# Performance work log

Hardware: AMD Instinct MI355X
Metric: run time of the kernel (lower is better)

## Reference

```python
import jax, jax.numpy as jnp
import numpy as np

N_NODES = 100000
N_EDGES = 1600000
IN_F = 64
H1_F = 64
N_CLS = 16
NEG_SLOPE = 0.01  # F.leaky_relu default


def _sage_pool(x, src, dst, n_nodes, W_pool, b_pool, W_self, W_neigh, bias):
    """DGL SAGEConv with aggregator_type='pool'.
    msg = relu(x[src] @ W_pool + b_pool); pooled = max over in-edges per dst
    out = x @ W_self + pooled @ W_neigh + bias (empty segments pooled to 0)."""
    m = jax.nn.relu(x[src] @ W_pool + b_pool)                 # [E, d_in]
    pooled = jax.ops.segment_max(m, dst, num_segments=n_nodes)  # [N, d_in]
    deg = jax.ops.segment_sum(jnp.ones(dst.shape[0], x.dtype), dst,
                              num_segments=n_nodes)           # [N]
    pooled = jnp.where(deg[:, None] > 0, pooled, jnp.zeros((), x.dtype))
    return x @ W_self + pooled @ W_neigh + bias               # [N, d_out]


def setup_inputs() -> dict:
    key = jax.random.key(0)
    ks = jax.random.split(key, 12)
    sc_in = 1.0 / np.sqrt(IN_F)
    sc_h1 = 1.0 / np.sqrt(H1_F)
    inp = {
        "in_feat": jax.random.normal(ks[0], (N_NODES, IN_F), jnp.float32),
        "src": jax.random.randint(ks[1], (N_EDGES,), 0, N_NODES),
        "dst": jax.random.randint(ks[2], (N_EDGES,), 0, N_NODES),
        # layer 1 (in=64 -> out=64)
        "W_pool1": jax.random.normal(ks[3], (IN_F, IN_F), jnp.float32) * sc_in,
        "b_pool1": jnp.zeros((IN_F,), jnp.float32),
        "W_self1": jax.random.normal(ks[4], (IN_F, H1_F), jnp.float32) * sc_in,
        "W_neigh1": jax.random.normal(ks[5], (IN_F, H1_F), jnp.float32) * sc_in,
        "bias1": jnp.zeros((H1_F,), jnp.float32),
        # layer 2 (in=64 -> out=16)
        "W_pool2": jax.random.normal(ks[6], (H1_F, H1_F), jnp.float32) * sc_h1,
        "b_pool2": jnp.zeros((H1_F,), jnp.float32),
        "W_self2": jax.random.normal(ks[7], (H1_F, N_CLS), jnp.float32) * sc_h1,
        "W_neigh2": jax.random.normal(ks[8], (H1_F, N_CLS), jnp.float32) * sc_h1,
        "bias2": jnp.zeros((N_CLS,), jnp.float32),
    }
    return inp


def reference(in_feat, src, dst,
              W_pool1, b_pool1, W_self1, W_neigh1, bias1,
              W_pool2, b_pool2, W_self2, W_neigh2, bias2):
    n = in_feat.shape[0]
    h = _sage_pool(in_feat, src, dst, n, W_pool1, b_pool1, W_self1, W_neigh1, bias1)
    h = jnp.where(h >= 0, h, NEG_SLOPE * h)  # leaky_relu
    out = _sage_pool(h, src, dst, n, W_pool2, b_pool2, W_self2, W_neigh2, bias2)
    return out
```

## Files before the change

### kernel.cpp

```cpp
#include <hip/hip_runtime.h>
#include <cstddef>
#include <cstdint>

#define CAP 64
#define SCAP 40
#define CHUNK2 4096
#define PR 5632
#define HPR 2816

typedef _Float16 h2 __attribute__((ext_vector_type(2)));
static __device__ __forceinline__ h2 h2max(h2 a, h2 b) {
  return __builtin_elementwise_max(a, b);
}
static __device__ __forceinline__ h2 bch2(int u) { return __builtin_bit_cast(h2, u); }
static __device__ __forceinline__ int packrelu(float a, float b) {
  h2 t; t.x = (_Float16)fmaxf(a, 0.f); t.y = (_Float16)fmaxf(b, 0.f);
  return __builtin_bit_cast(int, t);
}
static __device__ __forceinline__ int packleaky(float a, float b) {
  float la = (a >= 0.f) ? a : 0.01f * a;
  float lb = (b >= 0.f) ? b : 0.01f * b;
  h2 t; t.x = (_Float16)la; t.y = (_Float16)lb;
  return __builtin_bit_cast(int, t);
}
static __device__ __forceinline__ float fdot2f(h2 a, h2 b, float c) {
#if __has_builtin(__builtin_amdgcn_fdot2)
  return __builtin_amdgcn_fdot2(a, b, c, false);
#else
  return c + (float)a.x * (float)b.x + (float)a.y * (float)b.y;
#endif
}

static __device__ __forceinline__ void stageW64(h2* dstLds,
                                                const float* __restrict__ W,
                                                int tid) {
  #pragma unroll
  for (int it = 0; it < 2; it++) {
    int idx = it * 256 + tid;
    int kp = idx >> 4;
    int c4 = idx & 15;
    float4 a = ((const float4*)(W + (2 * kp) * 64))[c4];
    float4 b = ((const float4*)(W + (2 * kp + 1) * 64))[c4];
    h2 h0; h0.x = (_Float16)a.x; h0.y = (_Float16)b.x;
    h2 h1; h1.x = (_Float16)a.y; h1.y = (_Float16)b.y;
    h2 hv; hv.x = (_Float16)a.z; hv.y = (_Float16)b.z;
    h2 h3; h3.x = (_Float16)a.w; h3.y = (_Float16)b.w;
    int4 o = make_int4(__builtin_bit_cast(int, h0), __builtin_bit_cast(int, h1),
                       __builtin_bit_cast(int, hv), __builtin_bit_cast(int, h3));
    *(int4*)(dstLds + kp * 64 + c4 * 4) = o;
  }
}

__global__ __launch_bounds__(256) void k_build(const int* __restrict__ src,
                                               const int* __restrict__ dst,
                                               unsigned int* __restrict__ pairs,
                                               int* __restrict__ cnt2,
                                               int E, int P, int NC,
                                               const float* __restrict__ X,
                                               const float* __restrict__ W,
                                               const float* __restrict__ bias,
                                               _Float16* __restrict__ Z, int n) {
  __shared__ __attribute__((aligned(16))) char smem[24576];
  int tid = threadIdx.x;
  if ((int)blockIdx.x < NC) {
    int* hcnt = (int*)smem;
    for (int p = tid; p < 512; p += 256) hcnt[p] = 0;
    __syncthreads();
    int chunk = blockIdx.x;
    int e0 = chunk * CHUNK2;
    unsigned int* pbase = pairs + (size_t)chunk * P * SCAP;
    #pragma unroll
    for (int k = 0; k < CHUNK2 / 256; k++) {
      int e = e0 + k * 256 + tid;
      if (e < E) {
        int d = dst[e], s = src[e];
        int p = d >> 8;
        int slot = atomicAdd(&hcnt[p], 1);
        if (slot < SCAP)
          pbase[p * SCAP + slot] = (unsigned)s | ((unsigned)(d & 255) << 17);
      }
    }
    __syncthreads();
    int* cbase = cnt2 + (size_t)chunk * P;
    for (int p = tid; p < P; p += 256) {
      int c = hcnt[p];
      cbase[p] = (c < SCAP) ? c : SCAP;
    }
    return;
  }
  h2* sW  = (h2*)smem;
  h2* sXT = (h2*)(smem + 8192);
  stageW64(sW, W, tid);
  int node0 = (blockIdx.x - NC) * 128;
  #pragma unroll
  for (int it = 0; it < 8; it++) {
    int idx = it * 256 + tid;
    int row = idx & 127, c4 = idx >> 7;
    int node = node0 + row;
    float4 v = make_float4(0.f, 0.f, 0.f, 0.f);
    if (node < n) v = ((const float4*)(X + (size_t)node * 64))[c4];
    h2 a; a.x = (_Float16)v.x; a.y = (_Float16)v.y;
    h2 d; d.x = (_Float16)v.z; d.y = (_Float16)v.w;
    sXT[(2 * c4 + 0) * 128 + row] = a;
    sXT[(2 * c4 + 1) * 128 + row] = d;
  }
  __syncthreads();
  int lane = tid & 63;
  int cg = tid >> 6;
  float acc0[16], acc1[16];
  #pragma unroll
  for (int c4 = 0; c4 < 4; c4++) {
    float4 bv = ((const float4*)bias)[cg * 4 + c4];
    acc0[c4 * 4 + 0] = bv.x; acc0[c4 * 4 + 1] = bv.y;
    acc0[c4 * 4 + 2] = bv.z; acc0[c4 * 4 + 3] = bv.w;
    acc1[c4 * 4 + 0] = bv.x; acc1[c4 * 4 + 1] = bv.y;
    acc1[c4 * 4 + 2] = bv.z; acc1[c4 * 4 + 3] = bv.w;
  }
  #pragma unroll 8
  for (int kp = 0; kp < 32; kp++) {
    h2 x0 = sXT[kp * 128 + lane];
    h2 x1 = sXT[kp * 128 + lane + 64];
    const int4* wq = (const int4*)(sW + kp * 64 + cg * 16);
    #pragma unroll
    for (int q4 = 0; q4 < 4; q4++) {
      int4 wv = wq[q4];
      h2 w0 = bch2(wv.x), w1 = bch2(wv.y), w2 = bch2(wv.z), w3 = bch2(wv.w);
      acc0[q4 * 4 + 0] = fdot2f(x0, w0, acc0[q4 * 4 + 0]);
      acc0[q4 * 4 + 1] = fdot2f(x0, w1, acc0[q4 * 4 + 1]);
      acc0[q4 * 4 + 2] = fdot2f(x0, w2, acc0[q4 * 4 + 2]);
      acc0[q4 * 4 + 3] = fdot2f(x0, w3, acc0[q4 * 4 + 3]);
      acc1[q4 * 4 + 0] = fdot2f(x1, w0, acc1[q4 * 4 + 0]);
      acc1[q4 * 4 + 1] = fdot2f(x1, w1, acc1[q4 * 4 + 1]);
      acc1[q4 * 4 + 2] = fdot2f(x1, w2, acc1[q4 * 4 + 2]);
      acc1[q4 * 4 + 3] = fdot2f(x1, w3, acc1[q4 * 4 + 3]);
    }
  }
  int nodeA = node0 + lane;
  int nodeB = node0 + lane + 64;
  if (nodeA < n) {
    int4 o0, o1;
    o0.x = packrelu(acc0[0], acc0[1]);   o0.y = packrelu(acc0[2], acc0[3]);
    o0.z = packrelu(acc0[4], acc0[5]);   o0.w = packrelu(acc0[6], acc0[7]);
    o1.x = packrelu(acc0[8], acc0[9]);   o1.y = packrelu(acc0[10], acc0[11]);
    o1.z = packrelu(acc0[12], acc0[13]); o1.w = packrelu(acc0[14], acc0[15]);
    char* rp = (char*)Z + (size_t)nodeA * 128 + cg * 32;
    ((int4*)rp)[0] = o0; ((int4*)rp)[1] = o1;
  }
  if (nodeB < n) {
    int4 o0, o1;
    o0.x = packrelu(acc1[0], acc1[1]);   o0.y = packrelu(acc1[2], acc1[3]);
    o0.z = packrelu(acc1[4], acc1[5]);   o0.w = packrelu(acc1[6], acc1[7]);
    o1.x = packrelu(acc1[8], acc1[9]);   o1.y = packrelu(acc1[10], acc1[11]);
    o1.z = packrelu(acc1[12], acc1[13]); o1.w = packrelu(acc1[14], acc1[15]);
    char* rp = (char*)Z + (size_t)nodeB * 128 + cg * 32;
    ((int4*)rp)[0] = o0; ((int4*)rp)[1] = o1;
  }
}

__global__ __launch_bounds__(256) void k_fill3(const unsigned int* __restrict__ pairs,
                                               const int* __restrict__ cnt2,
                                               int* __restrict__ rowcnt,
                                               int* __restrict__ bucket,
                                               int n, int NC, int P) {
  __shared__ int sbucket[128 * CAP];
  __shared__ int scnt[128];
  __shared__ int soff[256];
  __shared__ int scnt2[512];
  int tid = threadIdx.x;
  int p = blockIdx.x >> 1;
  int half = blockIdx.x & 1;
  if (tid < 128) scnt[tid] = 0;
  for (int c = tid; c < NC; c += 256) scnt2[c] = cnt2[(size_t)c * P + p];
  __syncthreads();
  int total = NC * SCAP;
  for (int t = tid; t < total; t += 256) {
    int chunk = t / SCAP;
    int slot = t - chunk * SCAP;
    if (slot < scnt2[chunk]) {
      unsigned int u = pairs[(size_t)chunk * P * SCAP + p * SCAP + slot];
      int dlow = (int)(u >> 17);
      if ((dlow >> 7) == half) {
        int s = (int)(u & 0x1FFFFu);
        int li = dlow & 127;
        int sl = atomicAdd(&scnt[li], 1);
        if (sl < CAP)
          sbucket[li * CAP + sl] = s;
      }
    }
  }
  __syncthreads();
  int c = 0;
  if (tid < 128) {
    c = scnt[tid];
    if (c > CAP) c = CAP;
  }
  int ca = (c + 3) & ~3;
  soff[tid] = (tid < 128) ? ca : 0;
  __syncthreads();
  #pragma unroll
  for (int off = 1; off < 256; off <<= 1) {
    int t = (tid >= off) ? soff[tid - off] : 0;
    __syncthreads();
    soff[tid] += t;
    __syncthreads();
  }
  if (tid < 128) {
    int local = soff[tid] - ca;
    int node = (p << 8) + (half << 7) + tid;
    int gbase = p * PR + half * HPR + local;
    if (node < n)
      rowcnt[node] = gbase | (c << 22);
    for (int j = 0; j < c; j += 4) {
      int4 v = *(const int4*)&sbucket[tid * CAP + j];
      *(int4*)&bucket[gbase + j] = v;
    }
  }
}

static __device__ __forceinline__ h2 gather_one(const char* zb,
                                                const int* __restrict__ bucket,
                                                int rc) {
  int c = rc >> 22;
  const int* bk = bucket + (rc & 0x3FFFFF);
  h2 acc = (h2)(_Float16)0;
  int j = 0;
  for (; j + 8 <= c; j += 8) {
    int4 a = *(const int4*)(bk + j);
    int4 d = *(const int4*)(bk + j + 4);
    int u0 = *(const int*)(zb + (size_t)a.x * 128);
    int u1 = *(const int*)(zb + (size_t)a.y * 128);
    int u2 = *(const int*)(zb + (size_t)a.z * 128);
    int u3 = *(const int*)(zb + (size_t)a.w * 128);
    int u4 = *(const int*)(zb + (size_t)d.x * 128);
    int u5 = *(const int*)(zb + (size_t)d.y * 128);
    int u6 = *(const int*)(zb + (size_t)d.z * 128);
    int u7 = *(const int*)(zb + (size_t)d.w * 128);
    h2 m0 = h2max(bch2(u0), bch2(u1));
    h2 m1 = h2max(bch2(u2), bch2(u3));
    h2 m2 = h2max(bch2(u4), bch2(u5));
    h2 m3 = h2max(bch2(u6), bch2(u7));
    acc = h2max(acc, h2max(h2max(m0, m1), h2max(m2, m3)));
  }
  if (j + 4 <= c) {
    int4 a = *(const int4*)(bk + j);
    int u0 = *(const int*)(zb + (size_t)a.x * 128);
    int u1 = *(const int*)(zb + (size_t)a.y * 128);
    int u2 = *(const int*)(zb + (size_t)a.z * 128);
    int u3 = *(const int*)(zb + (size_t)a.w * 128);
    acc = h2max(acc, h2max(h2max(bch2(u0), bch2(u1)), h2max(bch2(u2), bch2(u3))));
    j += 4;
  }
  if (j + 2 <= c) {
    int2 a = *(const int2*)(bk + j);
    int u0 = *(const int*)(zb + (size_t)a.x * 128);
    int u1 = *(const int*)(zb + (size_t)a.y * 128);
    acc = h2max(acc, h2max(bch2(u0), bch2(u1)));
    j += 2;
  }
  if (j < c) {
    int u0 = *(const int*)(zb + (size_t)bk[j] * 128);
    acc = h2max(acc, bch2(u0));
  }
  return acc;
}

__global__ __launch_bounds__(256) void k_gather2(const _Float16* __restrict__ Z,
                                                 const int* __restrict__ bucket,
                                                 const int* __restrict__ rowcnt,
                                                 _Float16* __restrict__ pooled, int n) {
  int t = blockIdx.x * 256 + threadIdx.x;
  int pairid = t >> 5;
  int sub = t & 31;
  int nA = pairid * 2;
  int nB = nA + 1;
  if (nA >= n) return;
  const char* zb = (const char*)Z + sub * 4;
  int rcA = rowcnt[nA];
  h2 accA, accB;
  if (nB < n) {
    int rcB = rowcnt[nB];
    accA = gather_one(zb, bucket, rcA);
    accB = gather_one(zb, bucket, rcB);
    *(int*)((char*)pooled + (size_t)nA * 128 + sub * 4) = __builtin_bit_cast(int, accA);
    *(int*)((char*)pooled + (size_t)nB * 128 + sub * 4) = __builtin_bit_cast(int, accB);
  } else {
    accA = gather_one(zb, bucket, rcA);
    *(int*)((char*)pooled + (size_t)nA * 128 + sub * 4) = __builtin_bit_cast(int, accA);
  }
}

__global__ __launch_bounds__(256) void k_hl(const float* __restrict__ X,
                                            const _Float16* __restrict__ P,
                                            const float* __restrict__ Ws,
                                            const float* __restrict__ Wn,
                                            const float* __restrict__ bias,
                                            const float* __restrict__ Wp2,
                                            const float* __restrict__ bp2,
                                            _Float16* __restrict__ H,
                                            _Float16* __restrict__ Z2, int n) {
  __shared__ __attribute__((aligned(16))) h2 sWs[32 * 64];
  __shared__ __attribute__((aligned(16))) h2 sWn[32 * 64];
  __shared__ __attribute__((aligned(16))) h2 sXT[32 * 128];
  __shared__ __attribute__((aligned(16))) h2 sPT[32 * 128];
  int tid = threadIdx.x;
  stageW64(sWs, Ws, tid);
  stageW64(sWn, Wn, tid);
  int node0 = blockIdx.x * 128;
  #pragma unroll
  for (int it = 0; it < 8; it++) {
    int idx = it * 256 + tid;
    int row = idx & 127, c4 = idx >> 7;
    int node = node0 + row;
    float4 v = make_float4(0.f, 0.f, 0.f, 0.f);
    if (node < n) v = ((const float4*)(X + (size_t)node * 64))[c4];
    h2 a; a.x = (_Float16)v.x; a.y = (_Float16)v.y;
    h2 d; d.x = (_Float16)v.z; d.y = (_Float16)v.w;
    sXT[(2 * c4 + 0) * 128 + row] = a;
    sXT[(2 * c4 + 1) * 128 + row] = d;
  }
  #pragma unroll
  for (int it = 0; it < 4; it++) {
    int idx = it * 256 + tid;
    int row = idx & 127, q = idx >> 7;
    int node = node0 + row;
    int4 u = make_int4(0, 0, 0, 0);
    if (node < n) u = ((const int4*)((const char*)P + (size_t)node * 128))[q];
    sPT[(4 * q + 0) * 128 + row] = bch2(u.x);
    sPT[(4 * q + 1) * 128 + row] = bch2(u.y);
    sPT[(4 * q + 2) * 128 + row] = bch2(u.z);
    sPT[(4 * q + 3) * 128 + row] = bch2(u.w);
  }
  __syncthreads();
  int lane = tid & 63;
  int cg = tid >> 6;
  float acc0[16], acc1[16];
  #pragma unroll
  for (int c4 = 0; c4 < 4; c4++) {
    float4 bv = ((const float4*)bias)[cg * 4 + c4];
    acc0[c4 * 4 + 0] = bv.x; acc0[c4 * 4 + 1] = bv.y;
    acc0[c4 * 4 + 2] = bv.z; acc0[c4 * 4 + 3] = bv.w;
    acc1[c4 * 4 + 0] = bv.x; acc1[c4 * 4 + 1] = bv.y;
    acc1[c4 * 4 + 2] = bv.z; acc1[c4 * 4 + 3] = bv.w;
  }
  #pragma unroll 8
  for (int kp = 0; kp < 32; kp++) {
    h2 x0 = sXT[kp * 128 + lane];
    h2 x1 = sXT[kp * 128 + lane + 64];
    h2 p0 = sPT[kp * 128 + lane];
    h2 p1 = sPT[kp * 128 + lane + 64];
    const int4* wsq = (const int4*)(sWs + kp * 64 + cg * 16);
    const int4* wnq = (const int4*)(sWn + kp * 64 + cg * 16);
    #pragma unroll
    for (int q4 = 0; q4 < 4; q4++) {
      int4 a = wsq[q4];
      int4 d = wnq[q4];
      h2 s0 = bch2(a.x), s1 = bch2(a.y), s2 = bch2(a.z), s3 = bch2(a.w);
      h2 n0 = bch2(d.x), n1 = bch2(d.y), n2 = bch2(d.z), n3 = bch2(d.w);
      acc0[q4 * 4 + 0] = fdot2f(x0, s0, acc0[q4 * 4 + 0]);
      acc0[q4 * 4 + 1] = fdot2f(x0, s1, acc0[q4 * 4 + 1]);
      acc0[q4 * 4 + 2] = fdot2f(x0, s2, acc0[q4 * 4 + 2]);
      acc0[q4 * 4 + 3] = fdot2f(x0, s3, acc0[q4 * 4 + 3]);
      acc0[q4 * 4 + 0] = fdot2f(p0, n0, acc0[q4 * 4 + 0]);
      acc0[q4 * 4 + 1] = fdot2f(p0, n1, acc0[q4 * 4 + 1]);
      acc0[q4 * 4 + 2] = fdot2f(p0, n2, acc0[q4 * 4 + 2]);
      acc0[q4 * 4 + 3] = fdot2f(p0, n3, acc0[q4 * 4 + 3]);
      acc1[q4 * 4 + 0] = fdot2f(x1, s0, acc1[q4 * 4 + 0]);
      acc1[q4 * 4 + 1] = fdot2f(x1, s1, acc1[q4 * 4 + 1]);
      acc1[q4 * 4 + 2] = fdot2f(x1, s2, acc1[q4 * 4 + 2]);
      acc1[q4 * 4 + 3] = fdot2f(x1, s3, acc1[q4 * 4 + 3]);
      acc1[q4 * 4 + 0] = fdot2f(p1, n0, acc1[q4 * 4 + 0]);
      acc1[q4 * 4 + 1] = fdot2f(p1, n1, acc1[q4 * 4 + 1]);
      acc1[q4 * 4 + 2] = fdot2f(p1, n2, acc1[q4 * 4 + 2]);
      acc1[q4 * 4 + 3] = fdot2f(p1, n3, acc1[q4 * 4 + 3]);
    }
  }
  int ha[8], hb[8];
  #pragma unroll
  for (int j = 0; j < 8; j++) {
    ha[j] = packleaky(acc0[2 * j], acc0[2 * j + 1]);
    hb[j] = packleaky(acc1[2 * j], acc1[2 * j + 1]);
  }
  int nodeA = node0 + lane;
  int nodeB = node0 + lane + 64;
  __syncthreads();
  #pragma unroll
  for (int j = 0; j < 8; j++) {
    sXT[(cg * 8 + j) * 128 + lane]      = bch2(ha[j]);
    sXT[(cg * 8 + j) * 128 + lane + 64] = bch2(hb[j]);
  }
  stageW64(sWs, Wp2, tid);
  if (nodeA < n) {
    char* rp = (char*)H + (size_t)nodeA * 128 + cg * 32;
    ((int4*)rp)[0] = make_int4(ha[0], ha[1], ha[2], ha[3]);
    ((int4*)rp)[1] = make_int4(ha[4], ha[5], ha[6], ha[7]);
  }
  if (nodeB < n) {
    char* rp = (char*)H + (size_t)nodeB * 128 + cg * 32;
    ((int4*)rp)[0] = make_int4(hb[0], hb[1], hb[2], hb[3]);
    ((int4*)rp)[1] = make_int4(hb[4], hb[5], hb[6], hb[7]);
  }
  __syncthreads();
  float c0[16], c1[16];
  #pragma unroll
  for (int c4 = 0; c4 < 4; c4++) {
    float4 bv = ((const float4*)bp2)[cg * 4 + c4];
    c0[c4 * 4 + 0] = bv.x; c0[c4 * 4 + 1] = bv.y;
    c0[c4 * 4 + 2] = bv.z; c0[c4 * 4 + 3] = bv.w;
    c1[c4 * 4 + 0] = bv.x; c1[c4 * 4 + 1] = bv.y;
    c1[c4 * 4 + 2] = bv.z; c1[c4 * 4 + 3] = bv.w;
  }
  #pragma unroll 8
  for (int kp = 0; kp < 32; kp++) {
    h2 x0 = sXT[kp * 128 + lane];
    h2 x1 = sXT[kp * 128 + lane + 64];
    const int4* wq = (const int4*)(sWs + kp * 64 + cg * 16);
    #pragma unroll
    for (int q4 = 0; q4 < 4; q4++) {
      int4 wv = wq[q4];
      h2 w0 = bch2(wv.x), w1 = bch2(wv.y), w2 = bch2(wv.z), w3 = bch2(wv.w);
      c0[q4 * 4 + 0] = fdot2f(x0, w0, c0[q4 * 4 + 0]);
      c0[q4 * 4 + 1] = fdot2f(x0, w1, c0[q4 * 4 + 1]);
      c0[q4 * 4 + 2] = fdot2f(x0, w2, c0[q4 * 4 + 2]);
      c0[q4 * 4 + 3] = fdot2f(x0, w3, c0[q4 * 4 + 3]);
      c1[q4 * 4 + 0] = fdot2f(x1, w0, c1[q4 * 4 + 0]);
      c1[q4 * 4 + 1] = fdot2f(x1, w1, c1[q4 * 4 + 1]);
      c1[q4 * 4 + 2] = fdot2f(x1, w2, c1[q4 * 4 + 2]);
      c1[q4 * 4 + 3] = fdot2f(x1, w3, c1[q4 * 4 + 3]);
    }
  }
  if (nodeA < n) {
    int4 o0, o1;
    o0.x = packrelu(c0[0], c0[1]);   o0.y = packrelu(c0[2], c0[3]);
    o0.z = packrelu(c0[4], c0[5]);   o0.w = packrelu(c0[6], c0[7]);
    o1.x = packrelu(c0[8], c0[9]);   o1.y = packrelu(c0[10], c0[11]);
    o1.z = packrelu(c0[12], c0[13]); o1.w = packrelu(c0[14], c0[15]);
    char* rp = (char*)Z2 + (size_t)nodeA * 128 + cg * 32;
    ((int4*)rp)[0] = o0; ((int4*)rp)[1] = o1;
  }
  if (nodeB < n) {
    int4 o0, o1;
    o0.x = packrelu(c1[0], c1[1]);   o0.y = packrelu(c1[2], c1[3]);
    o0.z = packrelu(c1[4], c1[5]);   o0.w = packrelu(c1[6], c1[7]);
    o1.x = packrelu(c1[8], c1[9]);   o1.y = packrelu(c1[10], c1[11]);
    o1.z = packrelu(c1[12], c1[13]); o1.w = packrelu(c1[14], c1[15]);
    char* rp = (char*)Z2 + (size_t)nodeB * 128 + cg * 32;
    ((int4*)rp)[0] = o0; ((int4*)rp)[1] = o1;
  }
}

__global__ __launch_bounds__(256) void k_gather_out(const _Float16* __restrict__ Z,
                                                    const int* __restrict__ bucket,
                                                    const int* __restrict__ rowcnt,
                                                    const _Float16* __restrict__ Hrow,
                                                    const float* __restrict__ Ws,
                                                    const float* __restrict__ Wn,
                                                    const float* __restrict__ bias,
                                                    float* __restrict__ OUT, int n) {
  __shared__ __attribute__((aligned(16))) h2 sWs[32 * 16];
  __shared__ __attribute__((aligned(16))) h2 sWn[32 * 16];
  __shared__ __attribute__((aligned(16))) h2 sH[8][32];
  __shared__ __attribute__((aligned(16))) h2 sP[8][32];
  __shared__ float sB[16];
  int tid = threadIdx.x;
  #pragma unroll
  for (int it = 0; it < 2; it++) {
    int idx = it * 256 + tid;
    int kp = idx >> 4, c = idx & 15;
    h2 t1, t2;
    t1.x = (_Float16)Ws[(2 * kp) * 16 + c];
    t1.y = (_Float16)Ws[(2 * kp + 1) * 16 + c];
    t2.x = (_Float16)Wn[(2 * kp) * 16 + c];
    t2.y = (_Float16)Wn[(2 * kp + 1) * 16 + c];
    sWs[kp * 16 + c] = t1;
    sWn[kp * 16 + c] = t2;
  }
  if (tid < 16) sB[tid] = bias[tid];
  int nodeBase = blockIdx.x * 8;
  if (tid < 64) {
    int nd = nodeBase + (tid >> 3);
    int q = tid & 7;
    int4 u = make_int4(0, 0, 0, 0);
    if (nd < n) u = ((const int4*)((const char*)Hrow + (size_t)nd * 128))[q];
    ((int4*)&sH[tid >> 3][0])[q] = u;
  }
  int en = tid >> 5;
  int node = nodeBase + en;
  int sub = tid & 31;
  h2 acc = (h2)(_Float16)0;
  if (node < n)
    acc = gather_one((const char*)Z + sub * 4, bucket, rowcnt[node]);
  sP[en][sub] = acc;
  __syncthreads();
  int col = tid & 15;
  int kh = (tid >> 4) & 1;
  float v = 0.f;
  #pragma unroll
  for (int j = 0; j < 16; j++) {
    int kp = kh * 16 + j;
    v = fdot2f(sH[en][kp], sWs[kp * 16 + col], v);
    v = fdot2f(sP[en][kp], sWn[kp * 16 + col], v);
  }
  v += __shfl_xor(v, 16);
  if (kh == 0 && node < n)
    OUT[(size_t)node * 16 + col] = v + sB[col];
}

extern "C" void kernel_launch(void* const* d_in, const int* in_sizes, int n_in,
                              void* d_out, int out_size, void* d_ws, size_t ws_size,
                              hipStream_t stream) {
  const float* X   = (const float*)d_in[0];
  const int*   src = (const int*)d_in[1];
  const int*   dst = (const int*)d_in[2];
  const float* Wp1 = (const float*)d_in[3];
  const float* bp1 = (const float*)d_in[4];
  const float* Ws1 = (const float*)d_in[5];
  const float* Wn1 = (const float*)d_in[6];
  const float* b1  = (const float*)d_in[7];
  const float* Wp2 = (const float*)d_in[8];
  const float* bp2 = (const float*)d_in[9];
  const float* Ws2 = (const float*)d_in[10];
  const float* Wn2 = (const float*)d_in[11];
  const float* b2  = (const float*)d_in[12];
  float* OUT = (float*)d_out;

  const int n = in_sizes[0] / 64;
  const int E = in_sizes[1];
  const int P = (n + 255) >> 8;
  const int NC = (E + CHUNK2 - 1) / CHUNK2;

  char* w = (char*)d_ws;
  auto alloc = [&](size_t bytes) -> char* {
    char* p = w;
    w += (bytes + 255) & ~(size_t)255;
    return p;
  };
  int*  rowcnt = (int*)alloc((size_t)n * 4);
  int*  bucket = (int*)alloc((size_t)P * PR * 4);
  int*  cnt2   = (int*)alloc((size_t)NC * P * 4);
  size_t pairs_b = (size_t)NC * P * SCAP * 4;
  size_t h_b     = (size_t)n * 64 * 2;
  char* ali = alloc(pairs_b > h_b ? pairs_b : h_b);
  unsigned int* pairs = (unsigned int*)ali;
  _Float16*     h16   = (_Float16*)ali;
  _Float16* zh     = (_Float16*)alloc((size_t)n * 64 * 2);
  _Float16* pooled = (_Float16*)alloc((size_t)n * 64 * 2);
  (void)ws_size; (void)n_in; (void)out_size;

  const int nbT  = (n + 127) / 128;
  const int nbG2 = (n * 16 + 255) / 256;
  const int nbG8 = (n + 7) / 8;

  k_build<<<NC + nbT, 256, 0, stream>>>(src, dst, pairs, cnt2, E, P, NC,
                                        X, Wp1, bp1, zh, n);
  k_fill3<<<2 * P, 256, 0, stream>>>(pairs, cnt2, rowcnt, bucket, n, NC, P);
  k_gather2<<<nbG2, 256, 0, stream>>>(zh, bucket, rowcnt, pooled, n);
  k_hl<<<nbT, 256, 0, stream>>>(X, pooled, Ws1, Wn1, b1, Wp2, bp2, h16, zh, n);
  k_gather_out<<<nbG8, 256, 0, stream>>>(zh, bucket, rowcnt, h16,
                                         Ws2, Wn2, b2, OUT, n);
}
```

Measured before the change: 181.9 us.

## Rewrite k_hl dense transforms with MFMA 16x16x32 f16 and swizzled LDS

Replaces the fdot2-based per-node matmuls in the layer-1 combine/layer-2 pool kernel with MFMA 16x16x32 f16 instructions. Activations and weights are staged row-major in XOR-swizzled LDS, and outputs go back through LDS so global stores are coalesced. The aim is to cut ALU-bound time in this kernel, at the cost of extra LDS round trips and scalar half stores. This kernel is one of several in the pipeline, so the effect on total time is limited.

```diff
diff --git a/kernel.cpp b/kernel.cpp
--- a/kernel.cpp
+++ b/kernel.cpp
@@ -9,18 +9,15 @@
 #define HPR 2816
 
 typedef _Float16 h2 __attribute__((ext_vector_type(2)));
+typedef _Float16 f16x8 __attribute__((ext_vector_type(8)));
+typedef float f32x4 __attribute__((ext_vector_type(4)));
+
 static __device__ __forceinline__ h2 h2max(h2 a, h2 b) {
   return __builtin_elementwise_max(a, b);
 }
 static __device__ __forceinline__ h2 bch2(int u) { return __builtin_bit_cast(h2, u); }
 static __device__ __forceinline__ int packrelu(float a, float b) {
   h2 t; t.x = (_Float16)fmaxf(a, 0.f); t.y = (_Float16)fmaxf(b, 0.f);
-  return __builtin_bit_cast(int, t);
-}
-static __device__ __forceinline__ int packleaky(float a, float b) {
-  float la = (a >= 0.f) ? a : 0.01f * a;
-  float lb = (b >= 0.f) ? b : 0.01f * b;
-  h2 t; t.x = (_Float16)la; t.y = (_Float16)lb;
   return __builtin_bit_cast(int, t);
 }
 static __device__ __forceinline__ float fdot2f(h2 a, h2 b, float c) {
@@ -48,6 +45,28 @@
     int4 o = make_int4(__builtin_bit_cast(int, h0), __builtin_bit_cast(int, h1),
                        __builtin_bit_cast(int, hv), __builtin_bit_cast(int, h3));
     *(int4*)(dstLds + kp * 64 + c4 * 4) = o;
+  }
+}
+
+static __device__ __forceinline__ f16x8 fragLd(const char* base, int row, int k0) {
+  return *(const f16x8*)(base + ((row * 128 + k0 * 2) ^ ((row & 7) << 4)));
+}
+static __device__ __forceinline__ void stageWT(char* dstLds,
+                                               const float* __restrict__ W,
+                                               int tid) {
+  #pragma unroll
+  for (int it = 0; it < 4; it++) {
+    int idx = it * 256 + tid;
+    int k = idx >> 4;
+    int c4 = idx & 15;
+    float4 wv = ((const float4*)(W + k * 64))[c4];
+    #pragma unroll
+    for (int j = 0; j < 4; j++) {
+      int col = c4 * 4 + j;
+      float val = (j == 0) ? wv.x : (j == 1) ? wv.y : (j == 2) ? wv.z : wv.w;
+      *(_Float16*)(dstLds + ((col * 128 + k * 2) ^ ((col & 7) << 4))) =
+          (_Float16)val;
+    }
   }
 }
 
@@ -298,13 +317,13 @@
                                             const float* __restrict__ bp2,
                                             _Float16* __restrict__ H,
                                             _Float16* __restrict__ Z2, int n) {
-  __shared__ __attribute__((aligned(16))) h2 sWs[32 * 64];
-  __shared__ __attribute__((aligned(16))) h2 sWn[32 * 64];
-  __shared__ __attribute__((aligned(16))) h2 sXT[32 * 128];
-  __shared__ __attribute__((aligned(16))) h2 sPT[32 * 128];
+  __shared__ __attribute__((aligned(16))) char sX[128 * 128];
+  __shared__ __attribute__((aligned(16))) char sP[128 * 128];
+  __shared__ __attribute__((aligned(16))) char sWsT[64 * 128];
+  __shared__ __attribute__((aligned(16))) char sWnT[64 * 128];
   int tid = threadIdx.x;
-  stageW64(sWs, Ws, tid);
-  stageW64(sWn, Wn, tid);
+  stageWT(sWsT, Ws, tid);
+  stageWT(sWnT, Wn, tid);
   int node0 = blockIdx.x * 128;
   #pragma unroll
   for (int it = 0; it < 8; it++) {
@@ -313,10 +332,10 @@
     int node = node0 + row;
     float4 v = make_float4(0.f, 0.f, 0.f, 0.f);
     if (node < n) v = ((const float4*)(X + (size_t)node * 64))[c4];
-    h2 a; a.x = (_Float16)v.x; a.y = (_Float16)v.y;
-    h2 d; d.x = (_Float16)v.z; d.y = (_Float16)v.w;
-    sXT[(2 * c4 + 0) * 128 + row] = a;
-    sXT[(2 * c4 + 1) * 128 + row] = d;
+    h2 lo; lo.x = (_Float16)v.x; lo.y = (_Float16)v.y;
+    h2 hi; hi.x = (_Float16)v.z; hi.y = (_Float16)v.w;
+    int2 pk = make_int2(__builtin_bit_cast(int, lo), __builtin_bit_cast(int, hi));
+    *(int2*)(sX + ((row * 128 + c4 * 8) ^ ((row & 7) << 4))) = pk;
   }
   #pragma unroll
   for (int it = 0; it < 4; it++) {
@@ -325,126 +344,104 @@
     int node = node0 + row;
     int4 u = make_int4(0, 0, 0, 0);
     if (node < n) u = ((const int4*)((const char*)P + (size_t)node * 128))[q];
-    sPT[(4 * q + 0) * 128 + row] = bch2(u.x);
-    sPT[(4 * q + 1) * 128 + row] = bch2(u.y);
-    sPT[(4 * q + 2) * 128 + row] = bch2(u.z);
-    sPT[(4 * q + 3) * 128 + row] = bch2(u.w);
-  }
-  __syncthreads();
-  int lane = tid & 63;
-  int cg = tid >> 6;
-  float acc0[16], acc1[16];
-  #pragma unroll
-  for (int c4 = 0; c4 < 4; c4++) {
-    float4 bv = ((const float4*)bias)[cg * 4 + c4];
-    acc0[c4 * 4 + 0] = bv.x; acc0[c4 * 4 + 1] = bv.y;
-    acc0[c4 * 4 + 2] = bv.z; acc0[c4 * 4 + 3] = bv.w;
-    acc1[c4 * 4 + 0] = bv.x; acc1[c4 * 4 + 1] = bv.y;
-    acc1[c4 * 4 + 2] = bv.z; acc1[c4 * 4 + 3] = bv.w;
-  }
-  #pragma unroll 8
-  for (int kp = 0; kp < 32; kp++) {
-    h2 x0 = sXT[kp * 128 + lane];
-    h2 x1 = sXT[kp * 128 + lane + 64];
-    h2 p0 = sPT[kp * 128 + lane];
-    h2 p1 = sPT[kp * 128 + lane + 64];
-    const int4* wsq = (const int4*)(sWs + kp * 64 + cg * 16);
-    const int4* wnq = (const int4*)(sWn + kp * 64 + cg * 16);
-    #pragma unroll
-    for (int q4 = 0; q4 < 4; q4++) {
-      int4 a = wsq[q4];
-      int4 d = wnq[q4];
-      h2 s0 = bch2(a.x), s1 = bch2(a.y), s2 = bch2(a.z), s3 = bch2(a.w);
-      h2 n0 = bch2(d.x), n1 = bch2(d.y), n2 = bch2(d.z), n3 = bch2(d.w);
-      acc0[q4 * 4 + 0] = fdot2f(x0, s0, acc0[q4 * 4 + 0]);
-      acc0[q4 * 4 + 1] = fdot2f(x0, s1, acc0[q4 * 4 + 1]);
-      acc0[q4 * 4 + 2] = fdot2f(x0, s2, acc0[q4 * 4 + 2]);
-      acc0[q4 * 4 + 3] = fdot2f(x0, s3, acc0[q4 * 4 + 3]);
-      acc0[q4 * 4 + 0] = fdot2f(p0, n0, acc0[q4 * 4 + 0]);
-      acc0[q4 * 4 + 1] = fdot2f(p0, n1, acc0[q4 * 4 + 1]);
-      acc0[q4 * 4 + 2] = fdot2f(p0, n2, acc0[q4 * 4 + 2]);
-      acc0[q4 * 4 + 3] = fdot2f(p0, n3, acc0[q4 * 4 + 3]);
-      acc1[q4 * 4 + 0] = fdot2f(x1, s0, acc1[q4 * 4 + 0]);
-      acc1[q4 * 4 + 1] = fdot2f(x1, s1, acc1[q4 * 4 + 1]);
-      acc1[q4 * 4 + 2] = fdot2f(x1, s2, acc1[q4 * 4 + 2]);
-      acc1[q4 * 4 + 3] = fdot2f(x1, s3, acc1[q4 * 4 + 3]);
-      acc1[q4 * 4 + 0] = fdot2f(p1, n0, acc1[q4 * 4 + 0]);
-      acc1[q4 * 4 + 1] = fdot2f(p1, n1, acc1[q4 * 4 + 1]);
-      acc1[q4 * 4 + 2] = fdot2f(p1, n2, acc1[q4 * 4 + 2]);
-      acc1[q4 * 4 + 3] = fdot2f(p1, n3, acc1[q4 * 4 + 3]);
-    }
-  }
-  int ha[8], hb[8];
-  #pragma unroll
-  for (int j = 0; j < 8; j++) {
-    ha[j] = packleaky(acc0[2 * j], acc0[2 * j + 1]);
-    hb[j] = packleaky(acc1[2 * j], acc1[2 * j + 1]);
-  }
-  int nodeA = node0 + lane;
-  int nodeB = node0 + lane + 64;
-  __syncthreads();
-  #pragma unroll
-  for (int j = 0; j < 8; j++) {
-    sXT[(cg * 8 + j) * 128 + lane]      = bch2(ha[j]);
-    sXT[(cg * 8 + j) * 128 + lane + 64] = bch2(hb[j]);
-  }
-  stageW64(sWs, Wp2, tid);
-  if (nodeA < n) {
-    char* rp = (char*)H + (size_t)nodeA * 128 + cg * 32;
-    ((int4*)rp)[0] = make_int4(ha[0], ha[1], ha[2], ha[3]);
-    ((int4*)rp)[1] = make_int4(ha[4], ha[5], ha[6], ha[7]);
-  }
-  if (nodeB < n) {
-    char* rp = (char*)H + (size_t)nodeB * 128 + cg * 32;
-    ((int4*)rp)[0] = make_int4(hb[0], hb[1], hb[2], hb[3]);
-    ((int4*)rp)[1] = make_int4(hb[4], hb[5], hb[6], hb[7]);
-  }
-  __syncthreads();
-  float c0[16], c1[16];
-  #pragma unroll
-  for (int c4 = 0; c4 < 4; c4++) {
-    float4 bv = ((const float4*)bp2)[cg * 4 + c4];
-    c0[c4 * 4 + 0] = bv.x; c0[c4 * 4 + 1] = bv.y;
-    c0[c4 * 4 + 2] = bv.z; c0[c4 * 4 + 3] = bv.w;
-    c1[c4 * 4 + 0] = bv.x; c1[c4 * 4 + 1] = bv.y;
-    c1[c4 * 4 + 2] = bv.z; c1[c4 * 4 + 3] = bv.w;
-  }
-  #pragma unroll 8
-  for (int kp = 0; kp < 32; kp++) {
-    h2 x0 = sXT[kp * 128 + lane];
-    h2 x1 = sXT[kp * 128 + lane + 64];
-    const int4* wq = (const int4*)(sWs + kp * 64 + cg * 16);
-    #pragma unroll
-    for (int q4 = 0; q4 < 4; q4++) {
-      int4 wv = wq[q4];
-      h2 w0 = bch2(wv.x), w1 = bch2(wv.y), w2 = bch2(wv.z), w3 = bch2(wv.w);
-      c0[q4 * 4 + 0] = fdot2f(x0, w0, c0[q4 * 4 + 0]);
-      c0[q4 * 4 + 1] = fdot2f(x0, w1, c0[q4 * 4 + 1]);
-      c0[q4 * 4 + 2] = fdot2f(x0, w2, c0[q4 * 4 + 2]);
-      c0[q4 * 4 + 3] = fdot2f(x0, w3, c0[q4 * 4 + 3]);
-      c1[q4 * 4 + 0] = fdot2f(x1, w0, c1[q4 * 4 + 0]);
-      c1[q4 * 4 + 1] = fdot2f(x1, w1, c1[q4 * 4 + 1]);
-      c1[q4 * 4 + 2] = fdot2f(x1, w2, c1[q4 * 4 + 2]);
-      c1[q4 * 4 + 3] = fdot2f(x1, w3, c1[q4 * 4 + 3]);
-    }
-  }
-  if (nodeA < n) {
-    int4 o0, o1;
-    o0.x = packrelu(c0[0], c0[1]);   o0.y = packrelu(c0[2], c0[3]);
-    o0.z = packrelu(c0[4], c0[5]);   o0.w = packrelu(c0[6], c0[7]);
-    o1.x = packrelu(c0[8], c0[9]);   o1.y = packrelu(c0[10], c0[11]);
-    o1.z = packrelu(c0[12], c0[13]); o1.w = packrelu(c0[14], c0[15]);
-    char* rp = (char*)Z2 + (size_t)nodeA * 128 + cg * 32;
-    ((int4*)rp)[0] = o0; ((int4*)rp)[1] = o1;
-  }
-  if (nodeB < n) {
-    int4 o0, o1;
-    o0.x = packrelu(c1[0], c1[1]);   o0.y = packrelu(c1[2], c1[3]);
-    o0.z = packrelu(c1[4], c1[5]);   o0.w = packrelu(c1[6], c1[7]);
-    o1.x = packrelu(c1[8], c1[9]);   o1.y = packrelu(c1[10], c1[11]);
-    o1.z = packrelu(c1[12], c1[13]); o1.w = packrelu(c1[14], c1[15]);
-    char* rp = (char*)Z2 + (size_t)nodeB * 128 + cg * 32;
-    ((int4*)rp)[0] = o0; ((int4*)rp)[1] = o1;
+    *(int4*)(sP + ((row * 128 + q * 16) ^ ((row & 7) << 4))) = u;
+  }
+  __syncthreads();
+  int l = tid & 63;
+  int wv_ = tid >> 6;
+  int wrow = wv_ * 32;
+  int colq = l & 15;
+  int kgrp = (l >> 4) * 8;
+  f32x4 acc[2][4];
+  #pragma unroll
+  for (int m = 0; m < 2; m++)
+    #pragma unroll
+    for (int nt = 0; nt < 4; nt++) {
+      float bv = bias[nt * 16 + colq];
+      acc[m][nt] = (f32x4){bv, bv, bv, bv};
+    }
+  #pragma unroll
+  for (int ks = 0; ks < 64; ks += 32) {
+    f16x8 xa0 = fragLd(sX, wrow + colq, ks + kgrp);
+    f16x8 xa1 = fragLd(sX, wrow + 16 + colq, ks + kgrp);
+    f16x8 pa0 = fragLd(sP, wrow + colq, ks + kgrp);
+    f16x8 pa1 = fragLd(sP, wrow + 16 + colq, ks + kgrp);
+    #pragma unroll
+    for (int nt = 0; nt < 4; nt++) {
+      f16x8 bs = fragLd(sWsT, nt * 16 + colq, ks + kgrp);
+      f16x8 bn = fragLd(sWnT, nt * 16 + colq, ks + kgrp);
+      acc[0][nt] = __builtin_amdgcn_mfma_f32_16x16x32_f16(xa0, bs, acc[0][nt], 0, 0, 0);
+      acc[1][nt] = __builtin_amdgcn_mfma_f32_16x16x32_f16(xa1, bs, acc[1][nt], 0, 0, 0);
+      acc[0][nt] = __builtin_amdgcn_mfma_f32_16x16x32_f16(pa0, bn, acc[0][nt], 0, 0, 0);
+      acc[1][nt] = __builtin_amdgcn_mfma_f32_16x16x32_f16(pa1, bn, acc[1][nt], 0, 0, 0);
+    }
+  }
+  __syncthreads();
+  int rbase = (l >> 4) * 4;
+  #pragma unroll
+  for (int m = 0; m < 2; m++)
+    #pragma unroll
+    for (int nt = 0; nt < 4; nt++)
+      #pragma unroll
+      for (int r = 0; r < 4; r++) {
+        int nl = wrow + m * 16 + rbase + r;
+        int col = nt * 16 + colq;
+        float hv = acc[m][nt][r];
+        hv = (hv >= 0.f) ? hv : 0.01f * hv;
+        *(_Float16*)(sX + ((nl * 128 + col * 2) ^ ((nl & 7) << 4))) = (_Float16)hv;
+      }
+  stageWT(sWsT, Wp2, tid);
+  __syncthreads();
+  #pragma unroll
+  for (int it = 0; it < 4; it++) {
+    int idx = it * 256 + tid;
+    int row = idx & 127, q = idx >> 7;
+    int node = node0 + row;
+    if (node < n) {
+      int4 u = *(const int4*)(sX + ((row * 128 + q * 16) ^ ((row & 7) << 4)));
+      ((int4*)((char*)H + (size_t)node * 128))[q] = u;
+    }
+  }
+  f32x4 acc2[2][4];
+  #pragma unroll
+  for (int m = 0; m < 2; m++)
+    #pragma unroll
+    for (int nt = 0; nt < 4; nt++) {
+      float bv = bp2[nt * 16 + colq];
+      acc2[m][nt] = (f32x4){bv, bv, bv, bv};
+    }
+  #pragma unroll
+  for (int ks = 0; ks < 64; ks += 32) {
+    f16x8 ha0 = fragLd(sX, wrow + colq, ks + kgrp);
+    f16x8 ha1 = fragLd(sX, wrow + 16 + colq, ks + kgrp);
+    #pragma unroll
+    for (int nt = 0; nt < 4; nt++) {
+      f16x8 b = fragLd(sWsT, nt * 16 + colq, ks + kgrp);
+      acc2[0][nt] = __builtin_amdgcn_mfma_f32_16x16x32_f16(ha0, b, acc2[0][nt], 0, 0, 0);
+      acc2[1][nt] = __builtin_amdgcn_mfma_f32_16x16x32_f16(ha1, b, acc2[1][nt], 0, 0, 0);
+    }
+  }
+  #pragma unroll
+  for (int m = 0; m < 2; m++)
+    #pragma unroll
+    for (int nt = 0; nt < 4; nt++)
+      #pragma unroll
+      for (int r = 0; r < 4; r++) {
+        int nl = wrow + m * 16 + rbase + r;
+        int col = nt * 16 + colq;
+        float zv = fmaxf(acc2[m][nt][r], 0.f);
+        *(_Float16*)(sP + ((nl * 128 + col * 2) ^ ((nl & 7) << 4))) = (_Float16)zv;
+      }
+  __syncthreads();
+  #pragma unroll
+  for (int it = 0; it < 4; it++) {
+    int idx = it * 256 + tid;
+    int row = idx & 127, q = idx >> 7;
+    int node = node0 + row;
+    if (node < n) {
+      int4 u = *(const int4*)(sP + ((row * 128 + q * 16) ^ ((row & 7) << 4)));
+      ((int4*)((char*)Z2 + (size_t)node * 128))[q] = u;
+    }
   }
 }
 
```

Result: faster. 166.2 us (-8.6%).
